# Performance work log

Measured on AMD Instinct MI355X. Metric: run time of the kernel, lower is better.

## Reference

```python
import jax, jax.numpy as jnp
import numpy as np

EMB = 384
HEADS = 6
QDIM = 64
DFF = 4 * EMB
EPS = 1e-5


def layer_norm(x, g, b):
    mu = jnp.mean(x, axis=-1, keepdims=True)
    var = jnp.mean((x - mu) ** 2, axis=-1, keepdims=True)
    return (x - mu) * jax.lax.rsqrt(var + EPS) * g + b


def setup_inputs() -> dict:
    key = jax.random.key(0)
    ks = jax.random.split(key, 12)
    s = EMB ** -0.5
    return {
        "x": jax.random.normal(ks[0], (32, 512, EMB), dtype=jnp.float32),
        "Wq": jax.random.normal(ks[1], (EMB, EMB), dtype=jnp.float32) * s,
        "Wk": jax.random.normal(ks[2], (EMB, EMB), dtype=jnp.float32) * s,
        "Wv": jax.random.normal(ks[3], (EMB, EMB), dtype=jnp.float32) * s,
        "Wp": jax.random.normal(ks[4], (EMB, EMB), dtype=jnp.float32) * s,
        "bp": jnp.zeros((EMB,), dtype=jnp.float32),
        "g1": jnp.ones((EMB,), dtype=jnp.float32),
        "b1": jnp.zeros((EMB,), dtype=jnp.float32),
        "g2": jnp.ones((EMB,), dtype=jnp.float32),
        "b2": jnp.zeros((EMB,), dtype=jnp.float32),
        "W1": jax.random.normal(ks[5], (EMB, DFF), dtype=jnp.float32) * s,
        "bf1": jnp.zeros((DFF,), dtype=jnp.float32),
        "W2": jax.random.normal(ks[6], (DFF, EMB), dtype=jnp.float32) * (DFF ** -0.5),
        "bf2": jnp.zeros((EMB,), dtype=jnp.float32),
    }


def reference(x, Wq, Wk, Wv, Wp, bp, g1, b1, g2, b2, W1, bf1, W2, bf2):
    B, T, C = x.shape
    # --- self-attention on ln1(x) ---
    h = layer_norm(x, g1, b1)
    q = (h @ Wq).reshape(B, T, HEADS, QDIM).transpose(0, 2, 1, 3)  # [B,H,T,D]
    k = (h @ Wk).reshape(B, T, HEADS, QDIM).transpose(0, 2, 1, 3)
    v = (h @ Wv).reshape(B, T, HEADS, QDIM).transpose(0, 2, 1, 3)
    aff = jnp.einsum('bhtd,bhsd->bhts', q, k) * (QDIM ** -0.5)  # [B,H,T,T]
    causal = jnp.tril(jnp.ones((T, T), dtype=bool))
    aff = jnp.where(causal, aff, -jnp.inf)
    aff = jax.nn.softmax(aff, axis=-1)
    o = jnp.einsum('bhts,bhsd->bhtd', aff, v)
    o = o.transpose(0, 2, 1, 3).reshape(B, T, C)
    x = x + (o @ Wp + bp)
    # --- feed-forward on ln2(x) ---
    h2 = layer_norm(x, g2, b2)
    ff = jax.nn.relu(h2 @ W1 + bf1) @ W2 + bf2
    return x + ff
```

## Files before the change

kernel.cpp:

```cpp
#include <hip/hip_runtime.h>
#include <cstdint>
#include <cstddef>

#define DEVINL __device__ __forceinline__

typedef short short8 __attribute__((ext_vector_type(8)));
typedef float f32x4 __attribute__((ext_vector_type(4)));
typedef unsigned short ushort;
typedef ushort u16x8 __attribute__((ext_vector_type(8)));
typedef ushort u16x4 __attribute__((ext_vector_type(4)));

DEVINL float bf2f(ushort u) {
  union { unsigned int i; float f; } v; v.i = ((unsigned int)u) << 16; return v.f;
}
DEVINL ushort f2bf(float f) {
  union { float f; unsigned int i; } v; v.f = f;
  unsigned int u = v.i;
  unsigned int r = u + 0x7fffu + ((u >> 16) & 1u);
  return (ushort)(r >> 16);
}

__global__ void transpose_k(const float* __restrict__ in, ushort* __restrict__ out,
                            int R, int C) {
  __shared__ float tile[32][33];
  int bx = blockIdx.x, by = blockIdx.y;
  int tx = threadIdx.x, ty = threadIdx.y;
  int x = bx * 32 + tx;
#pragma unroll
  for (int i = 0; i < 4; i++) {
    int y = by * 32 + ty + i * 8;
    tile[ty + i * 8][tx] = in[(size_t)y * C + x];
  }
  __syncthreads();
  int x2 = by * 32 + tx;
#pragma unroll
  for (int i = 0; i < 4; i++) {
    int y2 = bx * 32 + ty + i * 8;
    out[(size_t)y2 * R + x2] = f2bf(tile[tx][ty + i * 8]);
  }
}

__global__ __launch_bounds__(256) void ln_k(const float* __restrict__ x,
                                            const float* __restrict__ g,
                                            const float* __restrict__ b,
                                            ushort* __restrict__ out) {
  int wave = threadIdx.x >> 6;
  int lane = threadIdx.x & 63;
  int row = blockIdx.x * 4 + wave;
  const float* xr = x + (size_t)row * 384;
  float v[6];
#pragma unroll
  for (int j = 0; j < 3; j++) {
    float2 p = *(const float2*)(xr + lane * 2 + j * 128);
    v[2 * j] = p.x;
    v[2 * j + 1] = p.y;
  }
  float s = v[0] + v[1] + v[2] + v[3] + v[4] + v[5];
#pragma unroll
  for (int off = 32; off; off >>= 1) s += __shfl_xor(s, off);
  float mu = s * (1.0f / 384.0f);
  float s2 = 0.f;
#pragma unroll
  for (int j = 0; j < 6; j++) { float d = v[j] - mu; s2 += d * d; }
#pragma unroll
  for (int off = 32; off; off >>= 1) s2 += __shfl_xor(s2, off);
  float rs = rsqrtf(s2 * (1.0f / 384.0f) + 1e-5f);
  ushort* orow = out + (size_t)row * 384;
#pragma unroll
  for (int j = 0; j < 3; j++) {
    int c = lane * 2 + j * 128;
    float2 pg = *(const float2*)(g + c);
    float2 pb = *(const float2*)(b + c);
    float y0 = (v[2 * j] - mu) * rs * pg.x + pb.x;
    float y1 = (v[2 * j + 1] - mu) * rs * pg.y + pb.y;
    uint32_t po = (uint32_t)f2bf(y0) | ((uint32_t)f2bf(y1) << 16);
    *(uint32_t*)(orow + c) = po;
  }
}

template <int MODE, int TN>
__global__ __launch_bounds__(256) void gemm_k(
    const ushort* __restrict__ A, int K,
    const ushort* __restrict__ WTa, const ushort* __restrict__ WTb,
    const ushort* __restrict__ WTc,
    const float* __restrict__ bias, const float* residf,
    ushort* __restrict__ outa, ushort* __restrict__ outb,
    ushort* __restrict__ outc, float* outf) {
  constexpr int NJ = TN / 32;
  __shared__ ushort As[128][40];
  __shared__ ushort Bs[TN][40];
  int tid = threadIdx.x;
  int lane = tid & 63, wave = tid >> 6;
  int wm = wave & 1, wn = wave >> 1;
  int q4 = lane >> 4, ln16 = lane & 15;
  int rowBase = blockIdx.x * 128;
  int colBase = blockIdx.y * TN;

  const ushort* WT;
  if (MODE == 0) {
    int z = blockIdx.z;
    WT = (z == 0) ? WTa : (z == 1) ? WTb : WTc;
  } else {
    WT = WTa;
  }

  f32x4 acc[4][NJ];
#pragma unroll
  for (int i = 0; i < 4; i++)
#pragma unroll
    for (int j = 0; j < NJ; j++) acc[i][j] = (f32x4){0.f, 0.f, 0.f, 0.f};

  int sRow = tid >> 2;
  int sKg = (tid & 3) * 8;

  for (int kb = 0; kb < K; kb += 32) {
#pragma unroll
    for (int r2 = 0; r2 < 128; r2 += 64) {
      int row = sRow + r2;
      *(u16x8*)&As[row][sKg] = *(const u16x8*)&A[(size_t)(rowBase + row) * K + kb + sKg];
    }
#pragma unroll
    for (int r2 = 0; r2 < TN; r2 += 64) {
      int row = sRow + r2;
      *(u16x8*)&Bs[row][sKg] = *(const u16x8*)&WT[(size_t)(colBase + row) * K + kb + sKg];
    }
    __syncthreads();
    short8 af[4], bfr[NJ];
#pragma unroll
    for (int i = 0; i < 4; i++) af[i] = *(const short8*)&As[wm * 64 + i * 16 + ln16][q4 * 8];
#pragma unroll
    for (int j = 0; j < NJ; j++)
      bfr[j] = *(const short8*)&Bs[wn * (TN / 2) + j * 16 + ln16][q4 * 8];
#pragma unroll
    for (int i = 0; i < 4; i++)
#pragma unroll
      for (int j = 0; j < NJ; j++)
        acc[i][j] = __builtin_amdgcn_mfma_f32_16x16x32_bf16(af[i], bfr[j], acc[i][j], 0, 0, 0);
    __syncthreads();
  }

#pragma unroll
  for (int i = 0; i < 4; i++) {
#pragma unroll
    for (int j = 0; j < NJ; j++) {
      int row0 = rowBase + wm * 64 + i * 16 + q4 * 4;
      int col = colBase + wn * (TN / 2) + j * 16 + ln16;
      if (MODE == 0) {
        int z = blockIdx.z;
        if (z < 2) {
          ushort* o = (z == 0) ? outa : outb;
#pragma unroll
          for (int r = 0; r < 4; r++) {
            int row = row0 + r;
            int bb = row >> 9, t = row & 511, h = col >> 6, d = col & 63;
            o[(((size_t)(bb * 6 + h) * 512) + t) * 64 + d] = f2bf(acc[i][j][r]);
          }
        } else {
          int bb = row0 >> 9, t0 = row0 & 511, h = col >> 6, d = col & 63;
          u16x4 pk = {f2bf(acc[i][j][0]), f2bf(acc[i][j][1]), f2bf(acc[i][j][2]),
                      f2bf(acc[i][j][3])};
          *(u16x4*)&outc[(((size_t)(bb * 6 + h) * 64) + d) * 512 + t0] = pk;
        }
      } else if (MODE == 1) {
        float bcol = bias[col];
#pragma unroll
        for (int r = 0; r < 4; r++) {
          size_t idx = (size_t)(row0 + r) * 384 + col;
          outf[idx] = acc[i][j][r] + bcol + residf[idx];
        }
      } else {
        float bcol = bias[col];
#pragma unroll
        for (int r = 0; r < 4; r++) {
          size_t idx = (size_t)(row0 + r) * 1536 + col;
          float vv = acc[i][j][r] + bcol;
          outa[idx] = f2bf(vv > 0.f ? vv : 0.f);
        }
      }
    }
  }
}

__global__ __launch_bounds__(256) void attn_k(const ushort* __restrict__ qg,
                                              const ushort* __restrict__ kg,
                                              const ushort* __restrict__ vtg,
                                              ushort* __restrict__ outg) {
  __shared__ ushort Ks[64][88];
  __shared__ ushort VTs[64][88];
  __shared__ ushort Pw[4][16][88];
  int tid = threadIdx.x, lane = tid & 63, wave = tid >> 6;
  int qb = blockIdx.x;
  int bh = blockIdx.y;
  int quad = lane >> 4, ln16 = lane & 15;
  int q0 = qb * 64 + wave * 16;
  int t_row = q0 + ln16;

  const ushort* qp = qg + (size_t)bh * 512 * 64;
  const ushort* kp = kg + (size_t)bh * 512 * 64;
  const ushort* vp = vtg + (size_t)bh * 64 * 512;

  short8 bq0 = *(const short8*)&qp[(size_t)t_row * 64 + quad * 8];
  short8 bq1 = *(const short8*)&qp[(size_t)t_row * 64 + 32 + quad * 8];

  f32x4 O[4];
#pragma unroll
  for (int dt = 0; dt < 4; dt++) O[dt] = (f32x4){0.f, 0.f, 0.f, 0.f};
  float m_ = -3.0e38f, l_ = 0.f;

  const float SC = 0.125f * 1.44269504088896f;

  for (int s0 = 0; s0 <= qb * 64; s0 += 64) {
    {
      int r = tid >> 2;
      int c0 = (tid & 3) * 8;
#pragma unroll
      for (int p = 0; p < 2; p++) {
        int c = c0 + p * 32;
        *(u16x8*)&Ks[r][c] = *(const u16x8*)&kp[(size_t)(s0 + r) * 64 + c];
        *(u16x8*)&VTs[r][c] = *(const u16x8*)&vp[(size_t)r * 512 + s0 + c];
      }
    }
    __syncthreads();

    f32x4 St[4];
#pragma unroll
    for (int kt = 0; kt < 4; kt++) {
      short8 a0 = *(const short8*)&Ks[kt * 16 + ln16][quad * 8];
      short8 a1 = *(const short8*)&Ks[kt * 16 + ln16][32 + quad * 8];
      f32x4 z = (f32x4){0.f, 0.f, 0.f, 0.f};
      z = __builtin_amdgcn_mfma_f32_16x16x32_bf16(a0, bq0, z, 0, 0, 0);
      z = __builtin_amdgcn_mfma_f32_16x16x32_bf16(a1, bq1, z, 0, 0, 0);
      St[kt] = z;
    }
#pragma unroll
    for (int kt = 0; kt < 4; kt++)
#pragma unroll
      for (int r = 0; r < 4; r++) {
        int s_abs = s0 + kt * 16 + quad * 4 + r;
        float vv = St[kt][r] * SC;
        St[kt][r] = (s_abs <= t_row) ? vv : -3.0e38f;
      }
    float vm = St[0][0];
#pragma unroll
    for (int kt = 0; kt < 4; kt++)
#pragma unroll
      for (int r = 0; r < 4; r++) vm = fmaxf(vm, St[kt][r]);
    vm = fmaxf(vm, __shfl_xor(vm, 16));
    vm = fmaxf(vm, __shfl_xor(vm, 32));
    float mn = fmaxf(m_, vm);
    float alpha = exp2f(m_ - mn);
    m_ = mn;
    float ps = 0.f;
#pragma unroll
    for (int kt = 0; kt < 4; kt++)
#pragma unroll
      for (int r = 0; r < 4; r++) {
        float p = exp2f(St[kt][r] - mn);
        St[kt][r] = p;
        ps += p;
      }
    ps += __shfl_xor(ps, 16);
    ps += __shfl_xor(ps, 32);
    l_ = l_ * alpha + ps;
#pragma unroll
    for (int dt = 0; dt < 4; dt++)
#pragma unroll
      for (int r = 0; r < 4; r++) O[dt][r] *= alpha;

#pragma unroll
    for (int kt = 0; kt < 4; kt++) {
      u16x4 pk = {f2bf(St[kt][0]), f2bf(St[kt][1]), f2bf(St[kt][2]), f2bf(St[kt][3])};
      *(u16x4*)&Pw[wave][ln16][kt * 16 + quad * 4] = pk;
    }
    asm volatile("" ::: "memory");
    union { u16x8 u; short8 s; } p0, p1;
    p0.u = *(const u16x8*)&Pw[wave][ln16][quad * 8];
    p1.u = *(const u16x8*)&Pw[wave][ln16][32 + quad * 8];
#pragma unroll
    for (int dt = 0; dt < 4; dt++) {
      short8 v0 = *(const short8*)&VTs[dt * 16 + ln16][quad * 8];
      short8 v1 = *(const short8*)&VTs[dt * 16 + ln16][32 + quad * 8];
      O[dt] = __builtin_amdgcn_mfma_f32_16x16x32_bf16(v0, p0.s, O[dt], 0, 0, 0);
      O[dt] = __builtin_amdgcn_mfma_f32_16x16x32_bf16(v1, p1.s, O[dt], 0, 0, 0);
    }
    __syncthreads();
  }

  float inv = 1.0f / l_;
  int b = bh / 6, h = bh % 6;
  size_t rowbase = ((size_t)(b * 512) + t_row) * 384 + h * 64;
#pragma unroll
  for (int dt = 0; dt < 4; dt++) {
    u16x4 pk = {f2bf(O[dt][0] * inv), f2bf(O[dt][1] * inv), f2bf(O[dt][2] * inv),
                f2bf(O[dt][3] * inv)};
    *(u16x4*)&outg[rowbase + dt * 16 + quad * 4] = pk;
  }
}

extern "C" void kernel_launch(void* const* d_in, const int* in_sizes, int n_in,
                              void* d_out, int out_size, void* d_ws, size_t ws_size,
                              hipStream_t stream) {
  const float* x = (const float*)d_in[0];
  const float* Wq = (const float*)d_in[1];
  const float* Wk = (const float*)d_in[2];
  const float* Wv = (const float*)d_in[3];
  const float* Wp = (const float*)d_in[4];
  const float* bp = (const float*)d_in[5];
  const float* g1 = (const float*)d_in[6];
  const float* b1 = (const float*)d_in[7];
  const float* g2 = (const float*)d_in[8];
  const float* b2 = (const float*)d_in[9];
  const float* W1 = (const float*)d_in[10];
  const float* bf1 = (const float*)d_in[11];
  const float* W2 = (const float*)d_in[12];
  const float* bf2 = (const float*)d_in[13];
  float* outp = (float*)d_out;

  char* ws = (char*)d_ws;
  size_t off = 0;
  auto alloc = [&](size_t elems) {
    ushort* p = (ushort*)(ws + off);
    off += elems * 2;
    return p;
  };
  ushort* WqT = alloc((size_t)384 * 384);
  ushort* WkT = alloc((size_t)384 * 384);
  ushort* WvT = alloc((size_t)384 * 384);
  ushort* WpT = alloc((size_t)384 * 384);
  ushort* W1T = alloc((size_t)384 * 1536);
  ushort* W2T = alloc((size_t)1536 * 384);
  ushort* bufq = alloc((size_t)16384 * 384);
  ushort* m1 = alloc((size_t)16384 * 1536);
  ushort* h1_attn = m1;
  ushort* bufk = m1 + (size_t)16384 * 384;
  ushort* vT = m1 + (size_t)2 * 16384 * 384;

  dim3 tb(32, 8);
  transpose_k<<<dim3(12, 12), tb, 0, stream>>>(Wq, WqT, 384, 384);
  transpose_k<<<dim3(12, 12), tb, 0, stream>>>(Wk, WkT, 384, 384);
  transpose_k<<<dim3(12, 12), tb, 0, stream>>>(Wv, WvT, 384, 384);
  transpose_k<<<dim3(12, 12), tb, 0, stream>>>(Wp, WpT, 384, 384);
  transpose_k<<<dim3(48, 12), tb, 0, stream>>>(W1, W1T, 384, 1536);
  transpose_k<<<dim3(12, 48), tb, 0, stream>>>(W2, W2T, 1536, 384);

  ln_k<<<4096, 256, 0, stream>>>(x, g1, b1, h1_attn);
  gemm_k<0, 128><<<dim3(128, 3, 3), 256, 0, stream>>>(
      h1_attn, 384, WqT, WkT, WvT, nullptr, nullptr, bufq, bufk, vT, nullptr);
  attn_k<<<dim3(8, 192), 256, 0, stream>>>(bufq, bufk, vT, h1_attn);
  gemm_k<1, 64><<<dim3(128, 6), 256, 0, stream>>>(
      h1_attn, 384, WpT, nullptr, nullptr, bp, x, nullptr, nullptr, nullptr, outp);
  ln_k<<<4096, 256, 0, stream>>>(outp, g2, b2, bufq);
  gemm_k<2, 128><<<dim3(128, 12), 256, 0, stream>>>(
      bufq, 384, W1T, nullptr, nullptr, bf1, nullptr, m1, nullptr, nullptr, nullptr);
  gemm_k<1, 64><<<dim3(128, 6), 256, 0, stream>>>(
      m1, 1536, W2T, nullptr, nullptr, bf2, outp, nullptr, nullptr, nullptr, outp);
}
```

Measured before the change: 295.4 us.

## Load GEMM tiles directly global-to-LDS with XOR swizzle; batch weight transposes

Result: faster. 280.8 us (-4.9%).

```diff
diff --git a/kernel.cpp b/kernel.cpp
--- a/kernel.cpp
+++ b/kernel.cpp
@@ -18,6 +18,37 @@
   unsigned int u = v.i;
   unsigned int r = u + 0x7fffu + ((u >> 16) & 1u);
   return (ushort)(r >> 16);
+}
+
+DEVINL void gl2lds16(const ushort* g, ushort* l) {
+  __builtin_amdgcn_global_load_lds(
+      (const __attribute__((address_space(1))) void*)g,
+      (__attribute__((address_space(3))) void*)l, 16, 0, 0);
+}
+
+__global__ void transpose4_k(const float* __restrict__ i0, const float* __restrict__ i1,
+                             const float* __restrict__ i2, const float* __restrict__ i3,
+                             ushort* __restrict__ o0, ushort* __restrict__ o1,
+                             ushort* __restrict__ o2, ushort* __restrict__ o3) {
+  __shared__ float tile[32][33];
+  int z = blockIdx.z;
+  const float* in = (z == 0) ? i0 : (z == 1) ? i1 : (z == 2) ? i2 : i3;
+  ushort* out = (z == 0) ? o0 : (z == 1) ? o1 : (z == 2) ? o2 : o3;
+  int bx = blockIdx.x, by = blockIdx.y;
+  int tx = threadIdx.x, ty = threadIdx.y;
+  int x = bx * 32 + tx;
+#pragma unroll
+  for (int i = 0; i < 4; i++) {
+    int y = by * 32 + ty + i * 8;
+    tile[ty + i * 8][tx] = in[(size_t)y * 384 + x];
+  }
+  __syncthreads();
+  int x2 = by * 32 + tx;
+#pragma unroll
+  for (int i = 0; i < 4; i++) {
+    int y2 = bx * 32 + ty + i * 8;
+    out[(size_t)y2 * 384 + x2] = f2bf(tile[tx][ty + i * 8]);
+  }
 }
 
 __global__ void transpose_k(const float* __restrict__ in, ushort* __restrict__ out,
@@ -87,8 +118,8 @@
     ushort* __restrict__ outa, ushort* __restrict__ outb,
     ushort* __restrict__ outc, float* outf) {
   constexpr int NJ = TN / 32;
-  __shared__ ushort As[128][40];
-  __shared__ ushort Bs[TN][40];
+  __shared__ __align__(16) ushort As[128 * 32];
+  __shared__ __align__(16) ushort Bs[TN * 32];
   int tid = threadIdx.x;
   int lane = tid & 63, wave = tid >> 6;
   int wm = wave & 1, wn = wave >> 1;
@@ -110,27 +141,33 @@
 #pragma unroll
     for (int j = 0; j < NJ; j++) acc[i][j] = (f32x4){0.f, 0.f, 0.f, 0.f};
 
-  int sRow = tid >> 2;
-  int sKg = (tid & 3) * 8;
+  int lr = lane >> 2;
+  int chunk = (lane & 3) ^ (lr & 3);
+  int rslot = (q4 ^ (ln16 & 3)) << 3;
 
   for (int kb = 0; kb < K; kb += 32) {
 #pragma unroll
-    for (int r2 = 0; r2 < 128; r2 += 64) {
-      int row = sRow + r2;
-      *(u16x8*)&As[row][sKg] = *(const u16x8*)&A[(size_t)(rowBase + row) * K + kb + sKg];
-    }
-#pragma unroll
-    for (int r2 = 0; r2 < TN; r2 += 64) {
-      int row = sRow + r2;
-      *(u16x8*)&Bs[row][sKg] = *(const u16x8*)&WT[(size_t)(colBase + row) * K + kb + sKg];
+    for (int h = 0; h < 128; h += 64) {
+      int base = wave * 16 + h;
+      gl2lds16(&A[(size_t)(rowBase + base + lr) * K + kb + chunk * 8], &As[base * 32]);
+    }
+#pragma unroll
+    for (int h = 0; h < TN; h += 64) {
+      int base = wave * 16 + h;
+      gl2lds16(&WT[(size_t)(colBase + base + lr) * K + kb + chunk * 8], &Bs[base * 32]);
     }
     __syncthreads();
     short8 af[4], bfr[NJ];
 #pragma unroll
-    for (int i = 0; i < 4; i++) af[i] = *(const short8*)&As[wm * 64 + i * 16 + ln16][q4 * 8];
-#pragma unroll
-    for (int j = 0; j < NJ; j++)
-      bfr[j] = *(const short8*)&Bs[wn * (TN / 2) + j * 16 + ln16][q4 * 8];
+    for (int i = 0; i < 4; i++) {
+      int ar = wm * 64 + i * 16 + ln16;
+      af[i] = *(const short8*)&As[ar * 32 + rslot];
+    }
+#pragma unroll
+    for (int j = 0; j < NJ; j++) {
+      int br = wn * (TN / 2) + j * 16 + ln16;
+      bfr[j] = *(const short8*)&Bs[br * 32 + rslot];
+    }
 #pragma unroll
     for (int i = 0; i < 4; i++)
 #pragma unroll
@@ -336,10 +373,7 @@
   ushort* vT = m1 + (size_t)2 * 16384 * 384;
 
   dim3 tb(32, 8);
-  transpose_k<<<dim3(12, 12), tb, 0, stream>>>(Wq, WqT, 384, 384);
-  transpose_k<<<dim3(12, 12), tb, 0, stream>>>(Wk, WkT, 384, 384);
-  transpose_k<<<dim3(12, 12), tb, 0, stream>>>(Wv, WvT, 384, 384);
-  transpose_k<<<dim3(12, 12), tb, 0, stream>>>(Wp, WpT, 384, 384);
+  transpose4_k<<<dim3(12, 12, 4), tb, 0, stream>>>(Wq, Wk, Wv, Wp, WqT, WkT, WvT, WpT);
   transpose_k<<<dim3(48, 12), tb, 0, stream>>>(W1, W1T, 384, 1536);
   transpose_k<<<dim3(12, 48), tb, 0, stream>>>(W2, W2T, 1536, 384);
 
```
